# Kernel tuning notes

Measured on AMD Instinct MI355X. Metric: run time of the kernel, lower is better.

The kernel has to match this reference:

```python
import math
import jax, jax.numpy as jnp
import numpy as np

B, N, C = 512, 196, 384
H, W = 14, 8  # rfft2 half-spectrum of 14x14 grid


def setup_inputs() -> dict:
    key = jax.random.key(0)
    k1, k2 = jax.random.split(key)
    x = jax.random.normal(k1, (B, N, C), dtype=jnp.float32)
    complex_weight = jax.random.normal(k2, (H, W, C, 2), dtype=jnp.float32) * 0.02
    return {"x": x, "complex_weight": complex_weight}


def reference(x, complex_weight):
    b_, n_, c_ = x.shape
    a = int(round(math.sqrt(n_)))  # spatial_size=None -> a = b = sqrt(N)
    xs = x.reshape(b_, a, a, c_).astype(jnp.float32)
    xf = jnp.fft.rfft2(xs, axes=(1, 2), norm="ortho")  # [B, a, a//2+1, C] complex
    w = jax.lax.complex(complex_weight[..., 0], complex_weight[..., 1])
    xf = xf * w
    out = jnp.fft.irfft2(xf, s=(a, a), axes=(1, 2), norm="ortho")
    return out.reshape(b_, n_, c_)
```

## Files before the change

### kernel.cpp

```cpp
#include <hip/hip_runtime.h>

namespace {
constexpr int Bb = 512, Nn = 196, Cc = 384, CT = 16, TPB = 128;
constexpr int SST = 212;
constexpr int AST = 20;
constexpr int APS = CT * AST;
constexpr int USZ = 14 * APS;

constexpr float C7t[7] = {1.f, 0.6234898018587335f, -0.2225209339563144f,
                          -0.9009688679024191f, -0.9009688679024191f,
                          -0.2225209339563144f, 0.6234898018587335f};
constexpr float S7t[7] = {0.f, 0.7818314824680298f, 0.9749279121818236f,
                          0.4338837391175581f, -0.4338837391175581f,
                          -0.9749279121818236f, -0.7818314824680298f};
constexpr float C14t[14] = {1.f, 0.9009688679024191f, 0.6234898018587336f, 0.2225209339563144f,
                            -0.2225209339563144f, -0.6234898018587336f, -0.9009688679024191f, -1.f,
                            -0.9009688679024191f, -0.6234898018587336f, -0.2225209339563144f,
                            0.2225209339563144f, 0.6234898018587336f, 0.9009688679024191f};
constexpr float S14t[14] = {0.f, 0.4338837391175581f, 0.7818314824680298f, 0.9749279121818236f,
                            0.9749279121818236f, 0.7818314824680298f, 0.4338837391175581f, 0.f,
                            -0.4338837391175581f, -0.7818314824680298f, -0.9749279121818236f,
                            -0.9749279121818236f, -0.7818314824680298f, -0.4338837391175581f};
}

template<int SG>
__device__ __forceinline__ void dft7(const float* vr, const float* vi, float* Er, float* Ei) {
  const float P1r = vr[1] + vr[6], M1r = vr[1] - vr[6];
  const float P1i = vi[1] + vi[6], M1i = vi[1] - vi[6];
  const float P2r = vr[2] + vr[5], M2r = vr[2] - vr[5];
  const float P2i = vi[2] + vi[5], M2i = vi[2] - vi[5];
  const float P3r = vr[3] + vr[4], M3r = vr[3] - vr[4];
  const float P3i = vi[3] + vi[4], M3i = vi[3] - vi[4];
  Er[0] = vr[0] + P1r + P2r + P3r;
  Ei[0] = vi[0] + P1i + P2i + P3i;
#pragma unroll
  for (int k = 1; k < 7; ++k) {
    const float c1 = C7t[k], c2 = C7t[(2 * k) % 7], c3 = C7t[(3 * k) % 7];
    const float s1 = SG * S7t[k], s2 = SG * S7t[(2 * k) % 7], s3 = SG * S7t[(3 * k) % 7];
    float er = fmaf(P1r, c1, vr[0]);
    er = fmaf(P2r, c2, er);
    er = fmaf(P3r, c3, er);
    er = fmaf(M1i, s1, er);
    er = fmaf(M2i, s2, er);
    er = fmaf(M3i, s3, er);
    float ei = fmaf(P1i, c1, vi[0]);
    ei = fmaf(P2i, c2, ei);
    ei = fmaf(P3i, c3, ei);
    ei = fmaf(M1r, -s1, ei);
    ei = fmaf(M2r, -s2, ei);
    ei = fmaf(M3r, -s3, ei);
    Er[k] = er; Ei[k] = ei;
  }
}

__global__ __launch_bounds__(TPB) void gf_kernel(const float* __restrict__ x,
                                                 const float* __restrict__ wt,
                                                 float* __restrict__ out) {
  __shared__ float U[USZ];
  __shared__ float Ct[14], St[14];

  const int tid = threadIdx.x;
  const int b   = blockIdx.x;
  const int c0  = blockIdx.y * CT;

  if (tid < 14) { Ct[tid] = C14t[tid]; St[tid] = S14t[tid]; }

  const float* xb = x + (size_t)b * (Nn * Cc) + c0;
  for (int i = tid; i < Nn * CT; i += TPB) {
    const int n = i >> 4, c = i & 15;
    U[c * SST + n] = xb[n * Cc + c];
  }
  __syncthreads();

  const int cl = tid & 15;
  const int w  = tid >> 4;

  float cwv[14], swv[14];
  {
    int idx = 0;
#pragma unroll
    for (int v = 0; v < 14; ++v) {
      cwv[v] = Ct[idx]; swv[v] = St[idx];
      idx += w; if (idx >= 14) idx -= 14;
    }
  }

  float Vr[14], Vi[14];
#pragma unroll
  for (int u = 0; u < 14; ++u) { Vr[u] = 0.f; Vi[u] = 0.f; }
  const float* Srow = &U[cl * SST];
#pragma unroll
  for (int j = 0; j < 49; ++j) {
    const float4 qd = *reinterpret_cast<const float4*>(&Srow[4 * j]);
    const float sv[4] = {qd.x, qd.y, qd.z, qd.w};
#pragma unroll
    for (int t = 0; t < 4; ++t) {
      const int e = 4 * j + t;
      const int u = e / 14, v = e % 14;
      Vr[u] = fmaf(sv[t],  cwv[v], Vr[u]);
      Vi[u] = fmaf(sv[t], -swv[v], Vi[u]);
    }
  }

  const float2* wp = reinterpret_cast<const float2*>(wt) + ((size_t)w * Cc + c0 + cl);
  float2 wreg[14];
#pragma unroll
  for (int h = 0; h < 14; ++h) wreg[h] = wp[(size_t)h * (8 * Cc)];

  __syncthreads();

  float evr[7], evi[7], odr[7], odi[7];
#pragma unroll
  for (int t = 0; t < 7; ++t) {
    evr[t] = Vr[2 * t];     evi[t] = Vi[2 * t];
    odr[t] = Vr[2 * t + 1]; odi[t] = Vi[2 * t + 1];
  }
  float Er[7], Ei[7], Qr[7], Qi[7];
  dft7<1>(evr, evi, Er, Ei);
  dft7<1>(odr, odi, Qr, Qi);
  float Xr[14], Xi[14];
  Xr[0] = Er[0] + Qr[0]; Xi[0] = Ei[0] + Qi[0];
  Xr[7] = Er[0] - Qr[0]; Xi[7] = Ei[0] - Qi[0];
#pragma unroll
  for (int h = 1; h < 7; ++h) {
    const float c = C14t[h], s = S14t[h];
    const float Tr = fmaf(Qr[h], c,  Qi[h] * s);
    const float Ti = fmaf(Qi[h], c, -Qr[h] * s);
    Xr[h] = Er[h] + Tr;     Xi[h] = Ei[h] + Ti;
    Xr[h + 7] = Er[h] - Tr; Xi[h + 7] = Ei[h] - Ti;
  }

  const float scale = ((w == 0 || w == 7) ? 1.f : 2.f) / 196.f;
  float Yr[14], Yi[14];
#pragma unroll
  for (int h = 0; h < 14; ++h) {
    const float wr = wreg[h].x, wi = wreg[h].y;
    Yr[h] = (Xr[h] * wr - Xi[h] * wi) * scale;
    Yi[h] = (Xr[h] * wi + Xi[h] * wr) * scale;
  }

#pragma unroll
  for (int t = 0; t < 7; ++t) {
    evr[t] = Yr[2 * t];     evi[t] = Yi[2 * t];
    odr[t] = Yr[2 * t + 1]; odi[t] = Yi[2 * t + 1];
  }
  dft7<-1>(evr, evi, Er, Ei);
  dft7<-1>(odr, odi, Qr, Qi);
  float* Ap = &U[cl * AST + w];
  Ap[0 * APS]     = Er[0] + Qr[0];  Ap[0 * APS + 8] = Ei[0] + Qi[0];
  Ap[7 * APS]     = Er[0] - Qr[0];  Ap[7 * APS + 8] = Ei[0] - Qi[0];
#pragma unroll
  for (int p = 1; p < 7; ++p) {
    const float c = C14t[p], s = S14t[p];
    const float Tr = fmaf(Qr[p], c, -Qi[p] * s);
    const float Ti = fmaf(Qi[p], c,  Qr[p] * s);
    Ap[p * APS]           = Er[p] + Tr;  Ap[p * APS + 8]       = Ei[p] + Ti;
    Ap[(p + 7) * APS]     = Er[p] - Tr;  Ap[(p + 7) * APS + 8] = Ei[p] - Ti;
  }
  __syncthreads();

  float* ob = out + (size_t)b * (Nn * Cc) + c0;
  for (int e = tid; e < 14 * CT; e += TPB) {
    const int c2 = e & 15, p = e >> 4;
    const float* ap = &U[p * APS + c2 * AST];
    float a[16];
    *reinterpret_cast<float4*>(&a[0])  = *reinterpret_cast<const float4*>(&ap[0]);
    *reinterpret_cast<float4*>(&a[4])  = *reinterpret_cast<const float4*>(&ap[4]);
    *reinterpret_cast<float4*>(&a[8])  = *reinterpret_cast<const float4*>(&ap[8]);
    *reinterpret_cast<float4*>(&a[12]) = *reinterpret_cast<const float4*>(&ap[12]);
    float* op = ob + (p * 14) * Cc + c2;
    op[0]       = ((a[0] + a[7]) + (a[1] + a[2])) + ((a[3] + a[4]) + (a[5] + a[6]));
    op[7 * Cc]  = ((a[0] - a[7]) - (a[1] - a[2])) - ((a[3] - a[4]) + (a[5] - a[6]));
#pragma unroll
    for (int q = 1; q < 7; ++q) {
      float cs = (q & 1) ? (a[0] - a[7]) : (a[0] + a[7]);
      float ss = 0.f;
#pragma unroll
      for (int w2 = 1; w2 < 7; ++w2) {
        const float c = C14t[(w2 * q) % 14];
        const float s = S14t[(w2 * q) % 14];
        cs = fmaf(a[w2], c, cs);
        ss = fmaf(a[8 + w2], s, ss);
      }
      op[q * Cc]        = cs - ss;
      op[(14 - q) * Cc] = cs + ss;
    }
  }
}

extern "C" void kernel_launch(void* const* d_in, const int* in_sizes, int n_in,
                              void* d_out, int out_size, void* d_ws, size_t ws_size,
                              hipStream_t stream) {
  const float* x  = (const float*)d_in[0];
  const float* wt = (const float*)d_in[1];
  float* out      = (float*)d_out;
  dim3 grid(Bb, Cc / CT);
  gf_kernel<<<grid, TPB, 0, stream>>>(x, wt, out);
}
```

Baseline: 314.5 us.

## Exploit row-DFT symmetry, vectorize global loads, unify smem layout, swap grid order

The first-stage row DFT now pairs columns v and v+7 using the (-1)^w symmetry, which halves the FMAs in the forward column pass. Input is loaded with float4 global reads into a padded shared layout, and the same buffer with a 228-float row stride replaces the separate transposed layout used for the inverse stage. The grid is swapped so consecutive blocks walk the channels of one batch, launch bounds request 4 blocks, and the loops are fully unrolled. Costs include extra float4 shared-memory loads per row and possible bank conflicts from the scalar transposing shared stores.

```diff
diff --git a/kernel.cpp b/kernel.cpp
--- a/kernel.cpp
+++ b/kernel.cpp
@@ -2,10 +2,8 @@
 
 namespace {
 constexpr int Bb = 512, Nn = 196, Cc = 384, CT = 16, TPB = 128;
-constexpr int SST = 212;
-constexpr int AST = 20;
-constexpr int APS = CT * AST;
-constexpr int USZ = 14 * APS;
+constexpr int RST = 228;
+constexpr int USZ = CT * RST;
 
 constexpr float C7t[7] = {1.f, 0.6234898018587335f, -0.2225209339563144f,
                           -0.9009688679024191f, -0.9009688679024191f,
@@ -53,53 +51,72 @@
   }
 }
 
-__global__ __launch_bounds__(TPB) void gf_kernel(const float* __restrict__ x,
-                                                 const float* __restrict__ wt,
-                                                 float* __restrict__ out) {
+__global__ __launch_bounds__(TPB, 4) void gf_kernel(const float* __restrict__ x,
+                                                    const float* __restrict__ wt,
+                                                    float* __restrict__ out) {
   __shared__ float U[USZ];
   __shared__ float Ct[14], St[14];
 
   const int tid = threadIdx.x;
-  const int b   = blockIdx.x;
-  const int c0  = blockIdx.y * CT;
+  const int b   = blockIdx.y;
+  const int c0  = blockIdx.x * CT;
 
   if (tid < 14) { Ct[tid] = C14t[tid]; St[tid] = S14t[tid]; }
 
   const float* xb = x + (size_t)b * (Nn * Cc) + c0;
-  for (int i = tid; i < Nn * CT; i += TPB) {
-    const int n = i >> 4, c = i & 15;
-    U[c * SST + n] = xb[n * Cc + c];
+#pragma unroll
+  for (int k = 0; k < 7; ++k) {
+    const int i = tid + k * TPB;
+    if (i < Nn * 4) {
+      const int n = i >> 2, g = (i & 3) << 2;
+      const float4 q = *reinterpret_cast<const float4*>(&xb[n * Cc + g]);
+      const int u = n / 14;
+      float* Un = &U[n + 2 * u];
+      Un[(g + 0) * RST] = q.x;
+      Un[(g + 1) * RST] = q.y;
+      Un[(g + 2) * RST] = q.z;
+      Un[(g + 3) * RST] = q.w;
+    }
   }
   __syncthreads();
 
   const int cl = tid & 15;
   const int w  = tid >> 4;
 
-  float cwv[14], swv[14];
+  float cw[7], sw[7];
   {
-    int idx = 0;
-#pragma unroll
-    for (int v = 0; v < 14; ++v) {
-      cwv[v] = Ct[idx]; swv[v] = St[idx];
+    int idx = w;
+#pragma unroll
+    for (int v = 1; v < 7; ++v) {
+      cw[v] = Ct[idx]; sw[v] = St[idx];
       idx += w; if (idx >= 14) idx -= 14;
     }
   }
+  const float sg = (w & 1) ? -1.f : 1.f;
 
   float Vr[14], Vi[14];
-#pragma unroll
-  for (int u = 0; u < 14; ++u) { Vr[u] = 0.f; Vi[u] = 0.f; }
-  const float* Srow = &U[cl * SST];
-#pragma unroll
-  for (int j = 0; j < 49; ++j) {
-    const float4 qd = *reinterpret_cast<const float4*>(&Srow[4 * j]);
-    const float sv[4] = {qd.x, qd.y, qd.z, qd.w};
-#pragma unroll
-    for (int t = 0; t < 4; ++t) {
-      const int e = 4 * j + t;
-      const int u = e / 14, v = e % 14;
-      Vr[u] = fmaf(sv[t],  cwv[v], Vr[u]);
-      Vi[u] = fmaf(sv[t], -swv[v], Vi[u]);
-    }
+  const float* Srow = &U[cl * RST];
+#pragma unroll
+  for (int u = 0; u < 14; ++u) {
+    const float4 q0 = *reinterpret_cast<const float4*>(&Srow[u * 16 + 0]);
+    const float4 q1 = *reinterpret_cast<const float4*>(&Srow[u * 16 + 4]);
+    const float4 q2 = *reinterpret_cast<const float4*>(&Srow[u * 16 + 8]);
+    const float4 q3 = *reinterpret_cast<const float4*>(&Srow[u * 16 + 12]);
+    const float f0 = fmaf(sg, q1.w, q0.x);
+    const float f1 = fmaf(sg, q2.x, q0.y);
+    const float f2 = fmaf(sg, q2.y, q0.z);
+    const float f3 = fmaf(sg, q2.z, q0.w);
+    const float f4 = fmaf(sg, q2.w, q1.x);
+    const float f5 = fmaf(sg, q3.x, q1.y);
+    const float f6 = fmaf(sg, q3.y, q1.z);
+    float vr = f0, vi = 0.f;
+    vr = fmaf(f1, cw[1], vr); vi = fmaf(f1, -sw[1], vi);
+    vr = fmaf(f2, cw[2], vr); vi = fmaf(f2, -sw[2], vi);
+    vr = fmaf(f3, cw[3], vr); vi = fmaf(f3, -sw[3], vi);
+    vr = fmaf(f4, cw[4], vr); vi = fmaf(f4, -sw[4], vi);
+    vr = fmaf(f5, cw[5], vr); vi = fmaf(f5, -sw[5], vi);
+    vr = fmaf(f6, cw[6], vr); vi = fmaf(f6, -sw[6], vi);
+    Vr[u] = vr; Vi[u] = vi;
   }
 
   const float2* wp = reinterpret_cast<const float2*>(wt) + ((size_t)w * Cc + c0 + cl);
@@ -146,44 +163,46 @@
   }
   dft7<-1>(evr, evi, Er, Ei);
   dft7<-1>(odr, odi, Qr, Qi);
-  float* Ap = &U[cl * AST + w];
-  Ap[0 * APS]     = Er[0] + Qr[0];  Ap[0 * APS + 8] = Ei[0] + Qi[0];
-  Ap[7 * APS]     = Er[0] - Qr[0];  Ap[7 * APS + 8] = Ei[0] - Qi[0];
+  float* Ap = &U[cl * RST + w];
+  Ap[0]            = Er[0] + Qr[0];  Ap[8]            = Ei[0] + Qi[0];
+  Ap[7 * 16]       = Er[0] - Qr[0];  Ap[7 * 16 + 8]   = Ei[0] - Qi[0];
 #pragma unroll
   for (int p = 1; p < 7; ++p) {
     const float c = C14t[p], s = S14t[p];
     const float Tr = fmaf(Qr[p], c, -Qi[p] * s);
     const float Ti = fmaf(Qi[p], c,  Qr[p] * s);
-    Ap[p * APS]           = Er[p] + Tr;  Ap[p * APS + 8]       = Ei[p] + Ti;
-    Ap[(p + 7) * APS]     = Er[p] - Tr;  Ap[(p + 7) * APS + 8] = Ei[p] - Ti;
+    Ap[p * 16]           = Er[p] + Tr;  Ap[p * 16 + 8]       = Ei[p] + Ti;
+    Ap[(p + 7) * 16]     = Er[p] - Tr;  Ap[(p + 7) * 16 + 8] = Ei[p] - Ti;
   }
   __syncthreads();
 
   float* ob = out + (size_t)b * (Nn * Cc) + c0;
-  for (int e = tid; e < 14 * CT; e += TPB) {
-    const int c2 = e & 15, p = e >> 4;
-    const float* ap = &U[p * APS + c2 * AST];
-    float a[16];
-    *reinterpret_cast<float4*>(&a[0])  = *reinterpret_cast<const float4*>(&ap[0]);
-    *reinterpret_cast<float4*>(&a[4])  = *reinterpret_cast<const float4*>(&ap[4]);
-    *reinterpret_cast<float4*>(&a[8])  = *reinterpret_cast<const float4*>(&ap[8]);
-    *reinterpret_cast<float4*>(&a[12]) = *reinterpret_cast<const float4*>(&ap[12]);
-    float* op = ob + (p * 14) * Cc + c2;
-    op[0]       = ((a[0] + a[7]) + (a[1] + a[2])) + ((a[3] + a[4]) + (a[5] + a[6]));
-    op[7 * Cc]  = ((a[0] - a[7]) - (a[1] - a[2])) - ((a[3] - a[4]) + (a[5] - a[6]));
-#pragma unroll
-    for (int q = 1; q < 7; ++q) {
-      float cs = (q & 1) ? (a[0] - a[7]) : (a[0] + a[7]);
-      float ss = 0.f;
-#pragma unroll
-      for (int w2 = 1; w2 < 7; ++w2) {
-        const float c = C14t[(w2 * q) % 14];
-        const float s = S14t[(w2 * q) % 14];
-        cs = fmaf(a[w2], c, cs);
-        ss = fmaf(a[8 + w2], s, ss);
+#pragma unroll
+  for (int r = 0; r < 2; ++r) {
+    const int e = tid + r * TPB;
+    if (e < 14 * CT) {
+      const int c2 = e & 15, p = e >> 4;
+      const float* ap = &U[c2 * RST + p * 16];
+      float a[16];
+      *reinterpret_cast<float4*>(&a[0])  = *reinterpret_cast<const float4*>(&ap[0]);
+      *reinterpret_cast<float4*>(&a[4])  = *reinterpret_cast<const float4*>(&ap[4]);
+      *reinterpret_cast<float4*>(&a[8])  = *reinterpret_cast<const float4*>(&ap[8]);
+      *reinterpret_cast<float4*>(&a[12]) = *reinterpret_cast<const float4*>(&ap[12]);
+      float* op = ob + (p * 14) * Cc + c2;
+      op[0]       = ((a[0] + a[7]) + (a[1] + a[2])) + ((a[3] + a[4]) + (a[5] + a[6]));
+      op[7 * Cc]  = ((a[0] - a[7]) - (a[1] - a[2])) - ((a[3] - a[4]) + (a[5] - a[6]));
+#pragma unroll
+      for (int q = 1; q < 7; ++q) {
+        float cs = (q & 1) ? (a[0] - a[7]) : (a[0] + a[7]);
+        float ss = 0.f;
+#pragma unroll
+        for (int w2 = 1; w2 < 7; ++w2) {
+          cs = fmaf(a[w2], C14t[(w2 * q) % 14], cs);
+          ss = fmaf(a[8 + w2], S14t[(w2 * q) % 14], ss);
+        }
+        op[q * Cc]        = cs - ss;
+        op[(14 - q) * Cc] = cs + ss;
       }
-      op[q * Cc]        = cs - ss;
-      op[(14 - q) * Cc] = cs + ss;
     }
   }
 }
@@ -194,6 +213,6 @@
   const float* x  = (const float*)d_in[0];
   const float* wt = (const float*)d_in[1];
   float* out      = (float*)d_out;
-  dim3 grid(Bb, Cc / CT);
+  dim3 grid(Cc / CT, Bb);
   gf_kernel<<<grid, TPB, 0, stream>>>(x, wt, out);
 }
```

Result: no change. 312.4 us (-0.7%).
